# Kernel tuning notes

Hardware: AMD Instinct MI355X
Metric: run time of the kernel (lower is better)

## Reference

```python
import jax, jax.numpy as jnp
import numpy as np

# Hardcoded skeleton graph from the source module (V=15 nodes, 28 directed edges)
_SRC = np.array([0,2,4,1,3,5,6,8,10,7,9,11,13,12,2,4,14,3,5,14,8,10,13,9,11,13,12,13])
_DST = np.array([2,4,14,3,5,14,8,10,13,9,11,13,14,13,0,2,4,1,3,5,6,8,10,7,9,11,13,14])
_V = 15

def _build_lhat():
    # PyG ChebConv norm with sym laplacian, lambda_max=2: L_hat = -D^{-1/2} A D^{-1/2}, diag 0
    A = np.zeros((_V, _V), np.float32)
    A[_DST, _SRC] = 1.0  # message flows src -> dst
    deg = A.sum(axis=1)
    dinv = np.where(deg > 0, deg ** -0.5, 0.0).astype(np.float32)
    return jnp.asarray(-(dinv[:, None] * A * dinv[None, :]))

_LHAT = _build_lhat()  # [V, V]

def _lstm_layer(xs, Wih, Whh, bih, bhh):
    # xs: [T, B, in]; torch LSTM gate order: i, f, g, o
    B = xs.shape[1]
    H = Whh.shape[1]
    b = bih + bhh
    def step(carry, xt):
        h, c = carry
        g = xt @ Wih.T + h @ Whh.T + b
        i, f, gg, o = jnp.split(g, 4, axis=-1)
        c = jax.nn.sigmoid(f) * c + jax.nn.sigmoid(i) * jnp.tanh(gg)
        h = jax.nn.sigmoid(o) * jnp.tanh(c)
        return (h, c), h
    init = (jnp.zeros((B, H), xs.dtype), jnp.zeros((B, H), xs.dtype))
    _, hs = jax.lax.scan(step, init, xs)
    return hs  # [T, B, H]

def setup_inputs() -> dict:
    key = jax.random.key(0)
    ks = jax.random.split(key, 16)
    N, C, T, V, M = 512, 3, 300, 15, 2
    H, IN, NC = 128, 45, 60
    s = 0.1
    return {
        "x1": jax.random.normal(ks[0], (N, C, T, V, M), jnp.float32),
        "x2": jax.random.normal(ks[1], (N, C, T, V, M), jnp.float32),
        "cheb_w0": jax.random.normal(ks[2], (3, 3), jnp.float32) * s,
        "cheb_w1": jax.random.normal(ks[3], (3, 3), jnp.float32) * s,
        "cheb_b": jax.random.normal(ks[4], (3,), jnp.float32) * s,
        "wih0": jax.random.normal(ks[5], (4 * H, IN), jnp.float32) * s,
        "whh0": jax.random.normal(ks[6], (4 * H, H), jnp.float32) * s,
        "bih0": jax.random.normal(ks[7], (4 * H,), jnp.float32) * s,
        "bhh0": jax.random.normal(ks[8], (4 * H,), jnp.float32) * s,
        "wih1": jax.random.normal(ks[9], (4 * H, H), jnp.float32) * s,
        "whh1": jax.random.normal(ks[10], (4 * H, H), jnp.float32) * s,
        "bih1": jax.random.normal(ks[11], (4 * H,), jnp.float32) * s,
        "bhh1": jax.random.normal(ks[12], (4 * H,), jnp.float32) * s,
        "fc_w": jax.random.normal(ks[13], (NC, H), jnp.float32) * np.sqrt(2.0 / NC).astype(np.float32),
        "fc_b": jax.random.normal(ks[14], (NC,), jnp.float32) * s,
    }

def reference(x1, x2, cheb_w0, cheb_w1, cheb_b, wih0, whh0, bih0, bhh0, wih1, whh1, bih1, bhh1, fc_w, fc_b):
    N, C, T, V, M = x1.shape
    # [N,C,T,V,M] -> [N*M*T, V, C]
    x = jnp.transpose(x1, (0, 4, 2, 3, 1)).reshape(N * M * T, V, C)
    # ChebConv K=2: out = Tx0 @ W0^T + Tx1 @ W1^T + b, Tx1 = L_hat @ x
    tx1 = jnp.einsum('ij,bjc->bic', _LHAT, x)
    x = x @ cheb_w0.T + tx1 @ cheb_w1.T + cheb_b
    # [N*M, T, V*C] -> time-major [T, N*M, V*C]
    seq = x.reshape(N * M, T, V * C).transpose(1, 0, 2)
    hs0 = _lstm_layer(seq, wih0, whh0, bih0, bhh0)
    hs1 = _lstm_layer(hs0, wih1, whh1, bih1, bhh1)
    h_last = hs1[-1]  # [N*M, 128]
    logits = h_last @ fc_w.T + fc_b
    return jax.nn.softmax(logits, axis=1)
```

## Files before the change

kernel.cpp:

```cpp
#include <hip/hip_runtime.h>
#include <hip/hip_fp16.h>

typedef _Float16 half_t;
typedef _Float16 half8 __attribute__((ext_vector_type(8)));
typedef float floatx4 __attribute__((ext_vector_type(4)));
typedef int   int4v  __attribute__((ext_vector_type(4)));

#define T_STEPS 300
#define NMB     1024
#define BS      16
#define NBLK    19

#define XP0   88
#define XROW0 (8*XP0 + 8)
#define HP    152
#define XROW1 (8*HP + 8)
#define HSLOT (8*HP)

#define XT_OFF   0ULL
#define XT_BYTES ((unsigned long long)(T_STEPS*NMB + 16)*64*2)
#define HS0_OFF  (XT_OFF + XT_BYTES)
#define HS0_BYTES ((unsigned long long)(T_STEPS*NMB + 16)*128*2)
#define WCH_OFF  (HS0_OFF + HS0_BYTES)
#define WCH_BYTES (512ULL*64*2)
#define BC_OFF   (WCH_OFF + WCH_BYTES)
#define BC_BYTES (512ULL*4)
#define FLAG_OFF (BC_OFF + BC_BYTES)

#define S2 0.70710678118654752f
#define QH 0.5f
#define UU 0.40824829046386302f
#define TH 0.33333333333333333f
__constant__ float LHAT[225] = {
  0,0,-S2,0,0,0,0,0,0,0,0,0,0,0,0,
  0,0,0,-S2,0,0,0,0,0,0,0,0,0,0,0,
  -S2,0,0,0,-QH,0,0,0,0,0,0,0,0,0,0,
  0,-S2,0,0,0,-QH,0,0,0,0,0,0,0,0,0,
  0,0,-QH,0,0,0,0,0,0,0,0,0,0,0,-UU,
  0,0,0,-QH,0,0,0,0,0,0,0,0,0,0,-UU,
  0,0,0,0,0,0,0,0,-S2,0,0,0,0,0,0,
  0,0,0,0,0,0,0,0,0,-S2,0,0,0,0,0,
  0,0,0,0,0,0,-S2,0,0,0,-QH,0,0,0,0,
  0,0,0,0,0,0,0,-S2,0,0,0,-QH,0,0,0,
  0,0,0,0,0,0,0,0,-QH,0,0,0,0,-UU,0,
  0,0,0,0,0,0,0,0,0,-QH,0,0,0,-UU,0,
  0,0,0,0,0,0,0,0,0,0,0,0,0,0,0,
  0,0,0,0,0,0,0,0,0,0,-UU,-UU,0,0,0,
  0,0,0,0,-UU,-UU,0,0,0,0,0,0,0,-TH,0
};

__device__ __forceinline__ float frcp(float x)  { return __builtin_amdgcn_rcpf(x); }
__device__ __forceinline__ float fsig(float x)  { return frcp(1.f + __expf(-x)); }
__device__ __forceinline__ float ftanh(float x) { return 2.f*frcp(1.f + __expf(-2.f*x)) - 1.f; }

__device__ __forceinline__ half8 load_w8(const float* p) {
  const float4* q = (const float4*)p;
  float4 a = q[0], b = q[1];
  half8 f;
  f[0]=(half_t)a.x; f[1]=(half_t)a.y; f[2]=(half_t)a.z; f[3]=(half_t)a.w;
  f[4]=(half_t)b.x; f[5]=(half_t)b.y; f[6]=(half_t)b.z; f[7]=(half_t)b.w;
  return f;
}

__device__ __forceinline__ void pin(half8& f) {
  int4v t = __builtin_bit_cast(int4v, f);
  asm volatile("" : "+v"(t));
  f = __builtin_bit_cast(half8, t);
}
__device__ __forceinline__ void pinf(floatx4& f) {
  int4v t = __builtin_bit_cast(int4v, f);
  asm volatile("" : "+v"(t));
  f = __builtin_bit_cast(floatx4, t);
}

__device__ __forceinline__ void wait_flag(const int* f, int want, int tid) {
  if (tid == 0) {
    while (__hip_atomic_load(f, __ATOMIC_RELAXED, __HIP_MEMORY_SCOPE_AGENT) < want)
      __builtin_amdgcn_s_sleep(8);
    (void)__hip_atomic_load(f, __ATOMIC_ACQUIRE, __HIP_MEMORY_SCOPE_AGENT);
  }
  __syncthreads();
}

__global__ void k_prep(const float* __restrict__ w0, const float* __restrict__ w1,
                       const float* __restrict__ cb, const float* __restrict__ wih0,
                       const float* __restrict__ bih0, const float* __restrict__ bhh0,
                       half_t* __restrict__ wcomb_h, float* __restrict__ biasc,
                       int* __restrict__ flags) {
  const int n = threadIdx.x;
  if (n < 256) flags[n*16] = 0;
  float wrow[45];
  #pragma unroll
  for (int i=0;i<45;i++) wrow[i] = wih0[n*45+i];
  float P[45];
  #pragma unroll
  for (int i=0;i<15;i++)
    #pragma unroll
    for (int c=0;c<3;c++) {
      float s = 0.f;
      #pragma unroll
      for (int cp=0;cp<3;cp++) s += wrow[i*3+cp]*w1[cp*3+c];
      P[i*3+c] = s;
    }
  #pragma unroll
  for (int j=0;j<15;j++)
    #pragma unroll
    for (int c=0;c<3;c++) {
      float s = 0.f;
      #pragma unroll
      for (int cp=0;cp<3;cp++) s += wrow[j*3+cp]*w0[cp*3+c];
      #pragma unroll
      for (int i=0;i<15;i++) s += LHAT[i*15+j]*P[i*3+c];
      wcomb_h[n*64 + j*3+c] = (half_t)s;
    }
  for (int k=45;k<64;k++) wcomb_h[n*64+k] = (half_t)0.f;
  float b = bih0[n] + bhh0[n];
  #pragma unroll
  for (int i=0;i<15;i++)
    #pragma unroll
    for (int cp=0;cp<3;cp++) b += wrow[i*3+cp]*cb[cp];
  biasc[n] = b;
}

__launch_bounds__(512, 1)
__global__ void k_lstm_fused(const float* __restrict__ x1, const half_t* __restrict__ wch,
                             const float* __restrict__ biasc, const float* __restrict__ whh0,
                             half_t* __restrict__ hs0,
                             const float* __restrict__ wih1, const float* __restrict__ whh1,
                             const float* __restrict__ bih1, const float* __restrict__ bhh1,
                             const float* __restrict__ fcw, const float* __restrict__ fcb,
                             float* __restrict__ out, int* __restrict__ flags) {
  __shared__ __align__(16) char smem[85120];
  half_t* S = (half_t*)smem;
  const int tid = threadIdx.x;
  const int wave = tid>>6, lane = tid&63, quad = lane>>4, l16 = lane&15;
  const int colw = wave*16 + l16;

  if (blockIdx.x < 128) {
    half_t* XS = S;
    half_t* HR = S + 2*BS*XROW0;
    const int wg  = blockIdx.x;
    const int nm0 = wg*8;
    const int n0t3 = wg*4*3;
    int* flag = flags + wg*16;

    for (int i=tid; i<2*BS*XROW0; i+=512) XS[i] = (half_t)0.f;
    for (int i=tid; i<HSLOT; i+=512) HR[15*HSLOT + i] = (half_t)0.f;

    half8 whhF[4][4]; half8 wcF[4][2]; floatx4 biasv[4];
    #pragma unroll
    for (int nt=0; nt<4; nt++) {
      const int gcol = nt*128 + colw;
      #pragma unroll
      for (int kc=0; kc<4; kc++) { whhF[nt][kc] = load_w8(whh0 + gcol*128 + kc*32 + quad*8); pin(whhF[nt][kc]); }
      #pragma unroll
      for (int kc=0; kc<2; kc++) { wcF[nt][kc] = *(const half8*)(wch + gcol*64 + kc*32 + quad*8); pin(wcF[nt][kc]); }
      const float b = biasc[gcol];
      biasv[nt] = (floatx4){b,b,b,b}; pinf(biasv[nt]);
    }
    float cst0 = 0.f, cst1 = 0.f;

    float2 xld[6];
    #define XLOAD(TBASE) { _Pragma("unroll") for (int k=0;k<6;k++) {          \
        const int idx=k*512+tid; const int v_=idx&15;                          \
        if (v_<15) { const int sh_=(idx>>4)&15; const int rB_=idx>>8;          \
          int tt=(TBASE)+sh_; if (tt>299) tt=299;                              \
          xld[k]=((const float2*)x1)[(size_t)((n0t3+rB_)*300+tt)*15+v_]; } } }
    #define XWRITE(BUFI) { _Pragma("unroll") for (int k=0;k<6;k++) {          \
        const int idx=k*512+tid; const int v_=idx&15;                          \
        if (v_<15) { const int sh_=(idx>>4)&15; const int rB_=idx>>8;          \
          const int nh_=rB_/3, c_=rB_-3*(rB_/3);                               \
          half_t* w = XS + ((BUFI)*BS + sh_)*XROW0 + nh_*2*XP0 + v_*3+c_;      \
          w[0]   = (half_t)xld[k].x;                                           \
          w[XP0] = (half_t)xld[k].y; } } }

    XLOAD(0); __syncthreads(); XWRITE(0);
    __syncthreads();

    for (int b=0; b<NBLK; b++) {
      const int bs = b*BS, buf = b&1;
      const int cnt = (T_STEPS - bs < BS) ? (T_STEPS - bs) : BS;
      const int ngr = cnt>>1;
      if (b+1 < NBLK) XLOAD(bs + BS);
      for (int g=0; g<ngr; g++) {
        const int s0 = g*2;
        floatx4 xp[4];
        {
          const half_t* xrow = XS + (buf*BS + s0 + (l16&1))*XROW0 + (l16>>1)*XP0;
          const half8 xa0 = *(const half8*)(xrow + quad*8);
          const half8 xa1 = *(const half8*)(xrow + 32 + quad*8);
          #pragma unroll
          for (int nt=0; nt<4; nt++) {
            floatx4 a = __builtin_amdgcn_mfma_f32_16x16x32_f16(xa0, wcF[nt][0], biasv[nt], 0,0,0);
            xp[nt]    = __builtin_amdgcn_mfma_f32_16x16x32_f16(xa1, wcF[nt][1], a, 0,0,0);
          }
        }
        #pragma unroll
        for (int js=0; js<2; js++) {
          const int t = bs + s0 + js;
          if (js==1 && g==0 && b+1 < NBLK) XWRITE(buf^1);
          floatx4 ah[4];
          {
            const half_t* hrow = HR + ((t+15)&15)*HSLOT + (l16>>1)*HP;
            half8 ha[4];
            #pragma unroll
            for (int kc=0; kc<4; kc++) ha[kc] = *(const half8*)(hrow + kc*32 + quad*8);
            #pragma unroll
            for (int nt=0; nt<4; nt++) {
              floatx4 a = __builtin_amdgcn_mfma_f32_16x16x32_f16(ha[0], whhF[nt][0], xp[nt], 0,0,0);
              a = __builtin_amdgcn_mfma_f32_16x16x32_f16(ha[1], whhF[nt][1], a, 0,0,0);
              a = __builtin_amdgcn_mfma_f32_16x16x32_f16(ha[2], whhF[nt][2], a, 0,0,0);
              ah[nt] = __builtin_amdgcn_mfma_f32_16x16x32_f16(ha[3], whhF[nt][3], a, 0,0,0);
            }
          }
          #pragma unroll
          for (int bb=0; bb<2; bb++) {
            const int r = bb*2 + js;
            float& cst = bb ? cst1 : cst0;
            cst = fsig(ah[1][r])*cst + fsig(ah[0][r])*ftanh(ah[2][r]);
            HR[(t&15)*HSLOT + (quad*2+bb)*HP + colw] = (half_t)(fsig(ah[3][r])*ftanh(cst));
          }
          __syncthreads();
        }
      }
      {
        const int hS = tid>>5, hR = (tid>>2)&7, hC = (tid&3)*32;
        if (hS < cnt) {
          half_t* dst = hs0 + ((size_t)(bs+hS)*NMB + nm0 + hR)*128 + hC;
          const half_t* src = HR + ((bs+hS)&15)*HSLOT + hR*HP + hC;
          #pragma unroll
          for (int k=0;k<4;k++) *(half8*)(dst + k*8) = *(const half8*)(src + k*8);
        }
      }
      __syncthreads();
      if (tid == 0)
        __hip_atomic_store(flag, b+1, __ATOMIC_RELEASE, __HIP_MEMORY_SCOPE_AGENT);
    }
  } else {
    half_t* XS = S;
    half_t* H2 = S + 2*BS*XROW1;
    float* logits_lds = (float*)(smem + (2*BS*XROW1 + 2*HSLOT)*2);
    const int wg  = blockIdx.x - 128;
    const int nm0 = wg*8;
    const int* flag = flags + wg*16;

    for (int i=tid; i<2*HSLOT; i+=512) H2[i] = (half_t)0.f;

    half8 whF[4][4], wxF[4][4]; floatx4 biasv[4];
    #pragma unroll
    for (int nt=0; nt<4; nt++) {
      const int gcol = nt*128 + colw;
      #pragma unroll
      for (int kc=0; kc<4; kc++) {
        wxF[nt][kc] = load_w8(wih1 + gcol*128 + kc*32 + quad*8); pin(wxF[nt][kc]);
        whF[nt][kc] = load_w8(whh1 + gcol*128 + kc*32 + quad*8); pin(whF[nt][kc]);
      }
      const float b = bih1[gcol] + bhh1[gcol];
      biasv[nt] = (floatx4){b,b,b,b}; pinf(biasv[nt]);
    }
    float cst0 = 0.f, cst1 = 0.f;

    const int sS = tid>>5, sR = (tid>>2)&7, sC = (tid&3)*32;
    const int coff = sS*XROW1 + sR*HP + sC;
    float4 ld[4];
    wait_flag(flag, 1, tid);
    { const half_t* src = hs0 + ((size_t)sS*NMB + nm0 + sR)*128 + sC;
      #pragma unroll
      for (int k=0;k<4;k++) ld[k] = *(const float4*)(src + k*8); }
    #pragma unroll
    for (int k=0;k<4;k++) *(half8*)(XS + coff + k*8) = __builtin_bit_cast(half8, ld[k]);
    __syncthreads();

    for (int b=0; b<NBLK; b++) {
      const int bs = b*BS, buf = b&1;
      const int cnt = (T_STEPS - bs < BS) ? (T_STEPS - bs) : BS;
      const int ngr = cnt>>1;
      if (b+1 < NBLK) {
        wait_flag(flag, b+2, tid);
        int tt = bs + BS + sS; if (tt > 299) tt = 299;
        const half_t* src = hs0 + ((size_t)tt*NMB + nm0 + sR)*128 + sC;
        #pragma unroll
        for (int k=0;k<4;k++) ld[k] = *(const float4*)(src + k*8);
      }
      for (int g=0; g<ngr; g++) {
        const int s0 = g*2;
        floatx4 xp[4];
        {
          const half_t* xrow = XS + (buf*BS + s0 + (l16&1))*XROW1 + (l16>>1)*HP;
          half8 xa[4];
          #pragma unroll
          for (int kc=0; kc<4; kc++) xa[kc] = *(const half8*)(xrow + kc*32 + quad*8);
          #pragma unroll
          for (int nt=0; nt<4; nt++) {
            floatx4 a = __builtin_amdgcn_mfma_f32_16x16x32_f16(xa[0], wxF[nt][0], biasv[nt], 0,0,0);
            a = __builtin_amdgcn_mfma_f32_16x16x32_f16(xa[1], wxF[nt][1], a, 0,0,0);
            a = __builtin_amdgcn_mfma_f32_16x16x32_f16(xa[2], wxF[nt][2], a, 0,0,0);
            xp[nt] = __builtin_amdgcn_mfma_f32_16x16x32_f16(xa[3], wxF[nt][3], a, 0,0,0);
          }
        }
        #pragma unroll
        for (int js=0; js<2; js++) {
          const int t = bs + s0 + js;
          if (js==1 && g==0 && b+1 < NBLK) {
            #pragma unroll
            for (int k=0;k<4;k++) *(half8*)(XS + ((buf^1)*BS)*XROW1 + coff + k*8) = __builtin_bit_cast(half8, ld[k]);
          }
          floatx4 ah[4];
          {
            const half_t* hrow = H2 + (t&1)*HSLOT + (l16>>1)*HP;
            half8 ha[4];
            #pragma unroll
            for (int kc=0; kc<4; kc++) ha[kc] = *(const half8*)(hrow + kc*32 + quad*8);
            #pragma unroll
            for (int nt=0; nt<4; nt++) {
              floatx4 a = __builtin_amdgcn_mfma_f32_16x16x32_f16(ha[0], whF[nt][0], xp[nt], 0,0,0);
              a = __builtin_amdgcn_mfma_f32_16x16x32_f16(ha[1], whF[nt][1], a, 0,0,0);
              a = __builtin_amdgcn_mfma_f32_16x16x32_f16(ha[2], whF[nt][2], a, 0,0,0);
              ah[nt] = __builtin_amdgcn_mfma_f32_16x16x32_f16(ha[3], whF[nt][3], a, 0,0,0);
            }
          }
          #pragma unroll
          for (int bb=0; bb<2; bb++) {
            const int r = bb*2 + js;
            float& cst = bb ? cst1 : cst0;
            cst = fsig(ah[1][r])*cst + fsig(ah[0][r])*ftanh(ah[2][r]);
            H2[((t+1)&1)*HSLOT + (quad*2+bb)*HP + colw] = (half_t)(fsig(ah[3][r])*ftanh(cst));
          }
          __syncthreads();
        }
      }
    }

    if (tid < 480) {
      const int rr = tid/60, cls = tid%60;
      float s = fcb[cls];
      for (int k2=0; k2<128; k2++) s += (float)H2[rr*HP + k2] * fcw[cls*128+k2];
      logits_lds[rr*60+cls] = s;
    }
    __syncthreads();
    if (tid < 8) {
      float m = -1e30f;
      for (int j=0; j<60; j++) m = fmaxf(m, logits_lds[tid*60+j]);
      float s = 0.f;
      for (int j=0; j<60; j++) s += __expf(logits_lds[tid*60+j]-m);
      const float inv = frcp(s);
      for (int j=0; j<60; j++) out[(nm0+tid)*60+j] = __expf(logits_lds[tid*60+j]-m)*inv;
    }
  }
}

extern "C" void kernel_launch(void* const* d_in, const int* in_sizes, int n_in,
                              void* d_out, int out_size, void* d_ws, size_t ws_size,
                              hipStream_t stream) {
  const float* x1      = (const float*)d_in[0];
  const float* cheb_w0 = (const float*)d_in[2];
  const float* cheb_w1 = (const float*)d_in[3];
  const float* cheb_b  = (const float*)d_in[4];
  const float* wih0    = (const float*)d_in[5];
  const float* whh0    = (const float*)d_in[6];
  const float* bih0    = (const float*)d_in[7];
  const float* bhh0    = (const float*)d_in[8];
  const float* wih1    = (const float*)d_in[9];
  const float* whh1    = (const float*)d_in[10];
  const float* bih1    = (const float*)d_in[11];
  const float* bhh1    = (const float*)d_in[12];
  const float* fc_w    = (const float*)d_in[13];
  const float* fc_b    = (const float*)d_in[14];

  char* ws = (char*)d_ws;
  half_t* hs0   = (half_t*)(ws + HS0_OFF);
  half_t* wch   = (half_t*)(ws + WCH_OFF);
  float*  biasc = (float*)(ws + BC_OFF);
  int*    flags = (int*)(ws + FLAG_OFF);

  k_prep<<<dim3(1), dim3(512), 0, stream>>>(cheb_w0, cheb_w1, cheb_b, wih0, bih0, bhh0, wch, biasc, flags);
  k_lstm_fused<<<dim3(256), dim3(512), 0, stream>>>(
      x1, wch, biasc, whh0, hs0, wih1, whh1, bih1, bhh1, fc_w, fc_b, (float*)d_out, flags);
}
```

Baseline: 429.0 us.

## Software-pipeline LSTM input projections one group ahead of the recurrence

Both LSTM layers now compute the input-projection MFMAs for the next pair of timesteps before running the recurrent steps of the current pair. Two register buffers hold the results and swap roles, and the group loop is unrolled by two so each group uses the buffer the previous one filled. This takes the input projection off the serial h-to-h dependency chain, so it can overlap with the recurrent matmuls and gate math. In exchange each thread holds an extra set of accumulator registers, which raises register pressure, and the final group of the last block does a wasted projection on unused data.

Result: no change. 426.0 us (-0.7%).

```diff
diff --git a/kernel.cpp b/kernel.cpp
--- a/kernel.cpp
+++ b/kernel.cpp
@@ -174,54 +174,57 @@
           w[0]   = (half_t)xld[k].x;                                           \
           w[XP0] = (half_t)xld[k].y; } } }
 
+    #define XP0COMP(DST, PTR) {                                                \
+      const half8 xa0 = *(const half8*)((PTR) + quad*8);                       \
+      const half8 xa1 = *(const half8*)((PTR) + 32 + quad*8);                  \
+      _Pragma("unroll") for (int nt=0; nt<4; nt++) {                           \
+        floatx4 a_ = __builtin_amdgcn_mfma_f32_16x16x32_f16(xa0, wcF[nt][0], biasv[nt], 0,0,0); \
+        DST[nt]    = __builtin_amdgcn_mfma_f32_16x16x32_f16(xa1, wcF[nt][1], a_, 0,0,0); } }
+
+    #define GROUP0(G, XPU, XPN) {                                              \
+      const int s0 = (G)*2;                                                    \
+      const int ns = s0+2;                                                     \
+      const half_t* nxrow = (ns < cnt)                                         \
+          ? XS + (buf*BS + ns + (l16&1))*XROW0 + (l16>>1)*XP0                  \
+          : XS + (((buf^1)*BS) + (l16&1))*XROW0 + (l16>>1)*XP0;                \
+      XP0COMP(XPN, nxrow);                                                     \
+      _Pragma("unroll") for (int js=0; js<2; js++) {                           \
+        const int t = bs + s0 + js;                                            \
+        if (js==1 && (G)==0 && b+1 < NBLK) XWRITE(buf^1);                      \
+        floatx4 ah[4];                                                         \
+        {                                                                      \
+          const half_t* hrow = HR + ((t+15)&15)*HSLOT + (l16>>1)*HP;           \
+          half8 ha[4];                                                         \
+          _Pragma("unroll") for (int kc=0; kc<4; kc++) ha[kc] = *(const half8*)(hrow + kc*32 + quad*8); \
+          _Pragma("unroll") for (int nt=0; nt<4; nt++) {                       \
+            floatx4 a_ = __builtin_amdgcn_mfma_f32_16x16x32_f16(ha[0], whhF[nt][0], XPU[nt], 0,0,0); \
+            a_ = __builtin_amdgcn_mfma_f32_16x16x32_f16(ha[1], whhF[nt][1], a_, 0,0,0); \
+            a_ = __builtin_amdgcn_mfma_f32_16x16x32_f16(ha[2], whhF[nt][2], a_, 0,0,0); \
+            ah[nt] = __builtin_amdgcn_mfma_f32_16x16x32_f16(ha[3], whhF[nt][3], a_, 0,0,0); } \
+        }                                                                      \
+        _Pragma("unroll") for (int bb=0; bb<2; bb++) {                         \
+          const int r = bb*2 + js;                                             \
+          float& cst = bb ? cst1 : cst0;                                       \
+          cst = fsig(ah[1][r])*cst + fsig(ah[0][r])*ftanh(ah[2][r]);           \
+          HR[(t&15)*HSLOT + (quad*2+bb)*HP + colw] = (half_t)(fsig(ah[3][r])*ftanh(cst)); \
+        }                                                                      \
+        __syncthreads();                                                       \
+      } }
+
     XLOAD(0); __syncthreads(); XWRITE(0);
     __syncthreads();
+
+    floatx4 xpA[4], xpB[4];
+    XP0COMP(xpA, XS + (l16&1)*XROW0 + (l16>>1)*XP0);
 
     for (int b=0; b<NBLK; b++) {
       const int bs = b*BS, buf = b&1;
       const int cnt = (T_STEPS - bs < BS) ? (T_STEPS - bs) : BS;
       const int ngr = cnt>>1;
       if (b+1 < NBLK) XLOAD(bs + BS);
-      for (int g=0; g<ngr; g++) {
-        const int s0 = g*2;
-        floatx4 xp[4];
-        {
-          const half_t* xrow = XS + (buf*BS + s0 + (l16&1))*XROW0 + (l16>>1)*XP0;
-          const half8 xa0 = *(const half8*)(xrow + quad*8);
-          const half8 xa1 = *(const half8*)(xrow + 32 + quad*8);
-          #pragma unroll
-          for (int nt=0; nt<4; nt++) {
-            floatx4 a = __builtin_amdgcn_mfma_f32_16x16x32_f16(xa0, wcF[nt][0], biasv[nt], 0,0,0);
-            xp[nt]    = __builtin_amdgcn_mfma_f32_16x16x32_f16(xa1, wcF[nt][1], a, 0,0,0);
-          }
-        }
-        #pragma unroll
-        for (int js=0; js<2; js++) {
-          const int t = bs + s0 + js;
-          if (js==1 && g==0 && b+1 < NBLK) XWRITE(buf^1);
-          floatx4 ah[4];
-          {
-            const half_t* hrow = HR + ((t+15)&15)*HSLOT + (l16>>1)*HP;
-            half8 ha[4];
-            #pragma unroll
-            for (int kc=0; kc<4; kc++) ha[kc] = *(const half8*)(hrow + kc*32 + quad*8);
-            #pragma unroll
-            for (int nt=0; nt<4; nt++) {
-              floatx4 a = __builtin_amdgcn_mfma_f32_16x16x32_f16(ha[0], whhF[nt][0], xp[nt], 0,0,0);
-              a = __builtin_amdgcn_mfma_f32_16x16x32_f16(ha[1], whhF[nt][1], a, 0,0,0);
-              a = __builtin_amdgcn_mfma_f32_16x16x32_f16(ha[2], whhF[nt][2], a, 0,0,0);
-              ah[nt] = __builtin_amdgcn_mfma_f32_16x16x32_f16(ha[3], whhF[nt][3], a, 0,0,0);
-            }
-          }
-          #pragma unroll
-          for (int bb=0; bb<2; bb++) {
-            const int r = bb*2 + js;
-            float& cst = bb ? cst1 : cst0;
-            cst = fsig(ah[1][r])*cst + fsig(ah[0][r])*ftanh(ah[2][r]);
-            HR[(t&15)*HSLOT + (quad*2+bb)*HP + colw] = (half_t)(fsig(ah[3][r])*ftanh(cst));
-          }
-          __syncthreads();
-        }
+      for (int g=0; g<ngr; g+=2) {
+        GROUP0(g,   xpA, xpB);
+        GROUP0(g+1, xpB, xpA);
       }
       {
         const int hS = tid>>5, hR = (tid>>2)&7, hC = (tid&3)*32;
@@ -263,6 +266,49 @@
     const int sS = tid>>5, sR = (tid>>2)&7, sC = (tid&3)*32;
     const int coff = sS*XROW1 + sR*HP + sC;
     float4 ld[4];
+
+    #define XP1COMP(DST, PTR) {                                                \
+      half8 xa[4];                                                             \
+      _Pragma("unroll") for (int kc=0; kc<4; kc++) xa[kc] = *(const half8*)((PTR) + kc*32 + quad*8); \
+      _Pragma("unroll") for (int nt=0; nt<4; nt++) {                           \
+        floatx4 a_ = __builtin_amdgcn_mfma_f32_16x16x32_f16(xa[0], wxF[nt][0], biasv[nt], 0,0,0); \
+        a_ = __builtin_amdgcn_mfma_f32_16x16x32_f16(xa[1], wxF[nt][1], a_, 0,0,0); \
+        a_ = __builtin_amdgcn_mfma_f32_16x16x32_f16(xa[2], wxF[nt][2], a_, 0,0,0); \
+        DST[nt] = __builtin_amdgcn_mfma_f32_16x16x32_f16(xa[3], wxF[nt][3], a_, 0,0,0); } }
+
+    #define GROUP1(G, XPU, XPN) {                                              \
+      const int s0 = (G)*2;                                                    \
+      const int ns = s0+2;                                                     \
+      const half_t* nxrow = (ns < cnt)                                         \
+          ? XS + (buf*BS + ns + (l16&1))*XROW1 + (l16>>1)*HP                   \
+          : XS + (((buf^1)*BS) + (l16&1))*XROW1 + (l16>>1)*HP;                 \
+      XP1COMP(XPN, nxrow);                                                     \
+      _Pragma("unroll") for (int js=0; js<2; js++) {                           \
+        const int t = bs + s0 + js;                                            \
+        if (js==1 && (G)==0 && b+1 < NBLK) {                                   \
+          _Pragma("unroll")                                                    \
+          for (int k=0;k<4;k++) *(half8*)(XS + ((buf^1)*BS)*XROW1 + coff + k*8) = __builtin_bit_cast(half8, ld[k]); \
+        }                                                                      \
+        floatx4 ah[4];                                                         \
+        {                                                                      \
+          const half_t* hrow = H2 + (t&1)*HSLOT + (l16>>1)*HP;                 \
+          half8 ha[4];                                                         \
+          _Pragma("unroll") for (int kc=0; kc<4; kc++) ha[kc] = *(const half8*)(hrow + kc*32 + quad*8); \
+          _Pragma("unroll") for (int nt=0; nt<4; nt++) {                       \
+            floatx4 a_ = __builtin_amdgcn_mfma_f32_16x16x32_f16(ha[0], whF[nt][0], XPU[nt], 0,0,0); \
+            a_ = __builtin_amdgcn_mfma_f32_16x16x32_f16(ha[1], whF[nt][1], a_, 0,0,0); \
+            a_ = __builtin_amdgcn_mfma_f32_16x16x32_f16(ha[2], whF[nt][2], a_, 0,0,0); \
+            ah[nt] = __builtin_amdgcn_mfma_f32_16x16x32_f16(ha[3], whF[nt][3], a_, 0,0,0); } \
+        }                                                                      \
+        _Pragma("unroll") for (int bb=0; bb<2; bb++) {                         \
+          const int r = bb*2 + js;                                             \
+          float& cst = bb ? cst1 : cst0;                                       \
+          cst = fsig(ah[1][r])*cst + fsig(ah[0][r])*ftanh(ah[2][r]);           \
+          H2[((t+1)&1)*HSLOT + (quad*2+bb)*HP + colw] = (half_t)(fsig(ah[3][r])*ftanh(cst)); \
+        }                                                                      \
+        __syncthreads();                                                       \
+      } }
+
     wait_flag(flag, 1, tid);
     { const half_t* src = hs0 + ((size_t)sS*NMB + nm0 + sR)*128 + sC;
       #pragma unroll
@@ -270,6 +316,9 @@
     #pragma unroll
     for (int k=0;k<4;k++) *(half8*)(XS + coff + k*8) = __builtin_bit_cast(half8, ld[k]);
     __syncthreads();
+
+    floatx4 xpA[4], xpB[4];
+    XP1COMP(xpA, XS + (l16&1)*XROW1 + (l16>>1)*HP);
 
     for (int b=0; b<NBLK; b++) {
       const int bs = b*BS, buf = b&1;
@@ -282,52 +331,9 @@
         #pragma unroll
         for (int k=0;k<4;k++) ld[k] = *(const float4*)(src + k*8);
       }
-      for (int g=0; g<ngr; g++) {
-        const int s0 = g*2;
-        floatx4 xp[4];
-        {
-          const half_t* xrow = XS + (buf*BS + s0 + (l16&1))*XROW1 + (l16>>1)*HP;
-          half8 xa[4];
-          #pragma unroll
-          for (int kc=0; kc<4; kc++) xa[kc] = *(const half8*)(xrow + kc*32 + quad*8);
-          #pragma unroll
-          for (int nt=0; nt<4; nt++) {
-            floatx4 a = __builtin_amdgcn_mfma_f32_16x16x32_f16(xa[0], wxF[nt][0], biasv[nt], 0,0,0);
-            a = __builtin_amdgcn_mfma_f32_16x16x32_f16(xa[1], wxF[nt][1], a, 0,0,0);
-            a = __builtin_amdgcn_mfma_f32_16x16x32_f16(xa[2], wxF[nt][2], a, 0,0,0);
-            xp[nt] = __builtin_amdgcn_mfma_f32_16x16x32_f16(xa[3], wxF[nt][3], a, 0,0,0);
-          }
-        }
-        #pragma unroll
-        for (int js=0; js<2; js++) {
-          const int t = bs + s0 + js;
-          if (js==1 && g==0 && b+1 < NBLK) {
-            #pragma unroll
-            for (int k=0;k<4;k++) *(half8*)(XS + ((buf^1)*BS)*XROW1 + coff + k*8) = __builtin_bit_cast(half8, ld[k]);
-          }
-          floatx4 ah[4];
-          {
-            const half_t* hrow = H2 + (t&1)*HSLOT + (l16>>1)*HP;
-            half8 ha[4];
-            #pragma unroll
-            for (int kc=0; kc<4; kc++) ha[kc] = *(const half8*)(hrow + kc*32 + quad*8);
-            #pragma unroll
-            for (int nt=0; nt<4; nt++) {
-              floatx4 a = __builtin_amdgcn_mfma_f32_16x16x32_f16(ha[0], whF[nt][0], xp[nt], 0,0,0);
-              a = __builtin_amdgcn_mfma_f32_16x16x32_f16(ha[1], whF[nt][1], a, 0,0,0);
-              a = __builtin_amdgcn_mfma_f32_16x16x32_f16(ha[2], whF[nt][2], a, 0,0,0);
-              ah[nt] = __builtin_amdgcn_mfma_f32_16x16x32_f16(ha[3], whF[nt][3], a, 0,0,0);
-            }
-          }
-          #pragma unroll
-          for (int bb=0; bb<2; bb++) {
-            const int r = bb*2 + js;
-            float& cst = bb ? cst1 : cst0;
-            cst = fsig(ah[1][r])*cst + fsig(ah[0][r])*ftanh(ah[2][r]);
-            H2[((t+1)&1)*HSLOT + (quad*2+bb)*HP + colw] = (half_t)(fsig(ah[3][r])*ftanh(cst));
-          }
-          __syncthreads();
-        }
+      for (int g=0; g<ngr; g+=2) {
+        GROUP1(g,   xpA, xpB);
+        GROUP1(g+1, xpB, xpA);
       }
     }
 
```
